# Optimization experiments

Measured on AMD Instinct MI355X. Metric: run time of the kernel, lower is better.

Reference implementation:

```python
import jax, jax.numpy as jnp
import numpy as np

FOCAL = 1015.0
IMG = 256


def setup_inputs() -> dict:
    key = jax.random.key(0)
    ks = jax.random.split(key, 9)
    B, NV, NF = 128, 35709, 70789
    coeff = jax.random.normal(ks[0], (B, 257), jnp.float32) * 0.1
    meanshape = jax.random.normal(ks[1], (NV * 3,), jnp.float32)
    idBase = jax.random.normal(ks[2], (NV * 3, 80), jnp.float32) * 0.01
    exBase = jax.random.normal(ks[3], (NV * 3, 64), jnp.float32) * 0.01
    meantex = jax.random.uniform(ks[4], (NV * 3,), jnp.float32) * 255.0
    texBase = jax.random.normal(ks[5], (NV * 3, 80), jnp.float32)
    # 1-based indices, matching the facemodel convention (code subtracts 1)
    tri = jax.random.randint(ks[6], (NF, 3), 1, NV + 1, jnp.int32)
    # point_buf may reference the appended zero face (index NF+1, 1-based)
    point_buf = jax.random.randint(ks[7], (NV, 8), 1, NF + 2, jnp.int32)
    kp_inds = jax.random.randint(ks[8], (68,), 0, NV, jnp.int32)
    return dict(coeff=coeff, meanshape=meanshape, idBase=idBase, exBase=exBase,
                meantex=meantex, texBase=texBase, tri=tri, point_buf=point_buf,
                kp_inds=kp_inds)


def _rotation(angles):
    # rotation = (Rz @ Ry @ Rx)^T, per Compute_rotation_matrix
    sx, sy, sz = jnp.sin(angles[:, 0]), jnp.sin(angles[:, 1]), jnp.sin(angles[:, 2])
    cx, cy, cz = jnp.cos(angles[:, 0]), jnp.cos(angles[:, 1]), jnp.cos(angles[:, 2])
    o, l = jnp.zeros_like(sx), jnp.ones_like(sx)
    Rx = jnp.stack([l, o, o, o, cx, -sx, o, sx, cx], -1).reshape(-1, 3, 3)
    Ry = jnp.stack([cy, o, sy, o, l, o, -sy, o, cy], -1).reshape(-1, 3, 3)
    Rz = jnp.stack([cz, -sz, o, sz, cz, o, o, o, l], -1).reshape(-1, 3, 3)
    return jnp.einsum('bij,bjk,bkl->bli', Rz, Ry, Rx)


def _compute_norm(shape, tri, point_buf):
    fid = tri - 1  # [F,3] 0-based vertex ids
    v1 = shape[:, fid[:, 0]]  # [B,F,3]
    v2 = shape[:, fid[:, 1]]
    v3 = shape[:, fid[:, 2]]
    fn = jnp.cross(v1 - v2, v2 - v3)  # per-face normals [B,F,3]
    fn = jnp.concatenate([fn, jnp.zeros_like(fn[:, :1])], axis=1)  # pad zero face
    vn = fn[:, point_buf - 1].sum(axis=2)  # [B,NV,8,3] -> [B,NV,3]
    return vn / jnp.linalg.norm(vn, axis=2, keepdims=True)


def _illumination(tex, norm, gamma):
    B, N, _ = tex.shape
    gamma = gamma.reshape(B, 3, 9).at[:, :, 0].add(0.8).transpose(0, 2, 1)  # [B,9,3]
    a0 = np.pi
    a1 = 2.0 * np.pi / np.sqrt(3.0)
    a2 = 2.0 * np.pi / np.sqrt(8.0)
    c0 = 1.0 / np.sqrt(4.0 * np.pi)
    c1 = np.sqrt(3.0) / np.sqrt(4.0 * np.pi)
    c2 = 3.0 * np.sqrt(5.0) / np.sqrt(12.0 * np.pi)
    d0 = 0.5 / np.sqrt(3.0)
    nx, ny, nz = norm[..., 0], norm[..., 1], norm[..., 2]
    Y = jnp.stack([
        jnp.full_like(nx, np.float32(a0 * c0)),
        -a1 * c1 * ny,
        a1 * c1 * nz,
        -a1 * c1 * nx,
        a2 * c2 * nx * ny,
        -a2 * c2 * ny * nz,
        a2 * c2 * d0 * (3.0 * nz ** 2 - 1.0),
        -a2 * c2 * nx * nz,
        a2 * c2 * 0.5 * (nx ** 2 - ny ** 2),
    ], axis=-1)  # [B,N,9]
    lighting = jnp.einsum('bnc,bcd->bnd', Y, gamma)  # [B,N,3]
    return tex * lighting


def _project(pts):
    half = IMG // 2
    pts = pts * jnp.array([1.0, 1.0, -1.0], jnp.float32) + jnp.array([0.0, 0.0, 10.0], jnp.float32)
    P = jnp.array([[FOCAL, 0.0, half], [0.0, FOCAL, half], [0.0, 0.0, 1.0]], jnp.float32)
    aug = pts @ P.T
    return aug[..., :2] / aug[..., 2:3]


def reference(coeff, meanshape, idBase, exBase, meantex, texBase, tri, point_buf, kp_inds):
    B = coeff.shape[0]
    idc, exc, texc = coeff[:, :80], coeff[:, 80:144], coeff[:, 144:224]
    angles, gamma, trans = coeff[:, 224:227], coeff[:, 227:254], coeff[:, 254:257]
    # Shape_formation
    shape = (idc @ idBase.T + exc @ exBase.T + meanshape).reshape(B, -1, 3)
    shape = shape - meanshape.reshape(1, -1, 3).mean(axis=1, keepdims=True)
    # Texture_formation
    tex = (texc @ texBase.T + meantex).reshape(B, -1, 3)
    # Normals, rotation, rigid transform
    vnorm = _compute_norm(shape, tri, point_buf)
    rot = _rotation(angles)  # [B,3,3]
    vnorm_r = jnp.einsum('bnc,bcd->bnd', vnorm, rot)
    shape_t = jnp.einsum('bnc,bcd->bnd', shape, rot) + trans[:, None, :]
    # Illumination (vertex colors) and landmark projection
    face_color = _illumination(tex, vnorm_r, gamma)
    lms = _project(shape_t[:, kp_inds])
    lms = jnp.stack([lms[..., 0], IMG - lms[..., 1]], axis=-1)
    return face_color, lms, shape_t
```

## Files before the change

kernel.cpp:

```cpp
#include <hip/hip_runtime.h>

typedef unsigned short u16;
typedef unsigned int u32;
typedef __attribute__((ext_vector_type(8))) short bfrag;
typedef __attribute__((ext_vector_type(4))) float ffrag;
typedef __attribute__((ext_vector_type(4))) float f4;
typedef __attribute__((ext_vector_type(2))) float f2;
typedef __attribute__((ext_vector_type(2))) u32 u32x2;
typedef __attribute__((ext_vector_type(4))) int i4;

#define NVERT 35709
#define NFACE 70789
#define NV3   107127
#define NB    128

#define SHAPE_OFF 0ull
#define TEX4_OFF  54849024ull
#define FXY_OFF   91415040ull
#define FZ_OFF    127659008ull
#define CPACK_OFF 145780992ull
#define MPAD_OFF  145846528ull
#define GG_OFF    145852672ull
#define MEAN_OFF  145866496ull
#define PART_OFF  145866512ull

#define LMS_BASE  13712256ull
#define ST_BASE   13729664ull

__device__ __forceinline__ float b2f(u16 s) {
  union { unsigned u; float f; } v; v.u = ((unsigned)s) << 16; return v.f;
}
__device__ __forceinline__ u16 f2b(float x) {
  union { float f; unsigned u; } v; v.f = x;
  unsigned r = v.u + 0x7FFFu + ((v.u >> 16) & 1u);
  return (u16)(r >> 16);
}
__device__ __forceinline__ u16 h2b(float x) {
  union { _Float16 h; u16 u; } v; v.h = (_Float16)x; return v.u;
}
__device__ __forceinline__ float hb2f(u16 u) {
  union { _Float16 h; u16 u2; } v; v.u2 = u; return (float)v.h;
}
__device__ __forceinline__ f4 ld4u(const float* p) {
  f4 r; __builtin_memcpy(&r, p, 16); return r;
}
__device__ __forceinline__ bfrag cvt8nt(const float* p) {
  f4 a = __builtin_nontemporal_load((const f4*)p);
  f4 b = __builtin_nontemporal_load((const f4*)(p + 4));
  bfrag r;
  r[0] = (short)f2b(a.x); r[1] = (short)f2b(a.y); r[2] = (short)f2b(a.z); r[3] = (short)f2b(a.w);
  r[4] = (short)f2b(b.x); r[5] = (short)f2b(b.y); r[6] = (short)f2b(b.z); r[7] = (short)f2b(b.w);
  return r;
}

__global__ __launch_bounds__(256) void k_mean(const float* __restrict__ ms, float* __restrict__ part) {
  __shared__ float s[3];
  if (threadIdx.x < 3) s[threadIdx.x] = 0.f;
  __syncthreads();
  float a0 = 0.f, a1 = 0.f, a2 = 0.f;
  for (int v = blockIdx.x * 256 + threadIdx.x; v < NVERT; v += 64 * 256) {
    a0 += ms[v * 3 + 0];
    a1 += ms[v * 3 + 1];
    a2 += ms[v * 3 + 2];
  }
  atomicAdd(&s[0], a0); atomicAdd(&s[1], a1); atomicAdd(&s[2], a2);
  __syncthreads();
  if (threadIdx.x < 3) part[blockIdx.x * 3 + threadIdx.x] = s[threadIdx.x];
}

__global__ __launch_bounds__(128) void k_params(const float* __restrict__ coeff, u16* __restrict__ cpack,
                                                float* __restrict__ mpad, float* __restrict__ G,
                                                const float* __restrict__ part, float* __restrict__ mean) {
  int b = threadIdx.x;
  if (b < 3) {
    float s = 0.f;
    for (int i = 0; i < 64; i++) s += part[i * 3 + b];
    mean[b] = s * (1.0f / (float)NVERT);
  }
  const float* c = coeff + b * 257;
  u16* cp = cpack + b * 256;
  for (int k = 0; k < 80; k++) cp[k] = f2b(c[k]);
  for (int k = 80; k < 96; k++) cp[k] = 0;
  for (int k = 0; k < 64; k++) cp[96 + k] = f2b(c[80 + k]);
  for (int k = 0; k < 80; k++) cp[160 + k] = f2b(c[144 + k]);
  for (int k = 240; k < 256; k++) cp[k] = 0;
  float ax = c[224], ay = c[225], az = c[226];
  float sx = sinf(ax), cx = cosf(ax);
  float sy = sinf(ay), cy = cosf(ay);
  float sz = sinf(az), cz = cosf(az);
  float* mp = mpad + b * 12;
  mp[0] = cz * cy;  mp[1] = cz * sy * sx - sz * cx;  mp[2] = sz * sx + cz * sy * cx;
  mp[3] = sz * cy;  mp[4] = cz * cx + sz * sy * sx;  mp[5] = sz * sy * cx - cz * sx;
  mp[6] = -sy;      mp[7] = cy * sx;                 mp[8] = cy * cx;
  mp[9] = c[254]; mp[10] = c[255]; mp[11] = c[256];
  float* g = G + b * 27;
  for (int cc = 0; cc < 9; cc++)
    for (int d = 0; d < 3; d++)
      g[cc * 3 + d] = c[227 + d * 9 + cc] + (cc == 0 ? 0.8f : 0.0f);
}

#define SBLK 558
__global__ __launch_bounds__(256) void k_gemmS(const float* __restrict__ idB, const float* __restrict__ exB,
                                               const float* __restrict__ ms, const u16* __restrict__ cpack,
                                               const float* __restrict__ meanc, const float* __restrict__ mpad,
                                               float* __restrict__ shp, float* __restrict__ out) {
  __shared__ float SW[4][2][384];
  int wave = threadIdx.x >> 6, lane = threadIdx.x & 63;
  int col = lane & 15, quad = lane >> 4;
  int jb = (blockIdx.x * 4 + wave) * 48;
  bfrag z8 = {0, 0, 0, 0, 0, 0, 0, 0};
  bfrag bid[3][3], bex[3][2];
  float msj[3], mcv[3];
#pragma unroll
  for (int T = 0; T < 3; T++) {
    int j = jb + T * 16 + col;
    int jc = j < NV3 ? j : NV3 - 1;
    const float* rowI = idB + (size_t)jc * 80;
    const float* rowE = exB + (size_t)jc * 64;
#pragma unroll
    for (int f = 0; f < 3; f++) {
      int k = f * 32 + quad * 8;
      bool ok = (k < 80);
      int ks = ok ? k : 0;
      bfrag vi = cvt8nt(rowI + ks);
      bid[T][f] = ok ? vi : z8;
    }
#pragma unroll
    for (int f = 0; f < 2; f++) bex[T][f] = cvt8nt(rowE + f * 32 + quad * 8);
    msj[T] = ms[jc];
    mcv[T] = meanc[jc % 3];
  }
  float (*SWl)[384] = SW[wave];
  int s0 = quad >> 1;
  int rb = (quad & 1) << 2;
  int vb = jb / 3;
  int ilim = NV3 - jb; ilim = (ilim > 48 ? 48 : ilim) * 8;
  int vlim = NVERT - vb; vlim = vlim > 16 ? 16 : vlim;

  for (int bt = 0; bt < 8; bt++) {
    const u16* cp = cpack + (size_t)(bt * 16 + col) * 256;
#pragma unroll
    for (int T = 0; T < 3; T++) {
      ffrag acc = {0.f, 0.f, 0.f, 0.f};
#pragma unroll
      for (int f = 0; f < 3; f++) {
        bfrag a = *(const bfrag*)(cp + f * 32 + quad * 8);
        acc = __builtin_amdgcn_mfma_f32_16x16x32_bf16(a, bid[T][f], acc, 0, 0, 0);
      }
#pragma unroll
      for (int f = 0; f < 2; f++) {
        bfrag a = *(const bfrag*)(cp + 96 + f * 32 + quad * 8);
        acc = __builtin_amdgcn_mfma_f32_16x16x32_bf16(a, bex[T][f], acc, 0, 0, 0);
      }
#pragma unroll
      for (int rr = 0; rr < 2; rr++) {
        f2 v2;
        v2.x = acc[2 * rr] + msj[T] - mcv[T];
        v2.y = acc[2 * rr + 1] + msj[T] - mcv[T];
        *(f2*)&SWl[s0][(T * 16 + col) * 8 + rb + 2 * rr] = v2;
      }
    }
#pragma unroll
    for (int s = 0; s < 2; s++) {
      size_t sb = (size_t)(bt * 2 + s) * (size_t)(NV3 * 8) + (size_t)jb * 8;
#pragma unroll
      for (int it = 0; it < 3; it++) {
        int i = it * 128 + lane * 2;
        if (i < ilim) {
          f2 vv = *(f2*)&SWl[s][i];
          __builtin_nontemporal_store(vv, (f2*)(shp + sb + i));
        }
      }
    }
#pragma unroll
    for (int s = 0; s < 2; s++) {
#pragma unroll
      for (int kk = 0; kk < 2; kk++) {
        int bi = (lane >> 4) + (kk << 2);
        int vloc = lane & 15;
        int b = bt * 16 + s * 8 + bi;
        float x = SWl[s][vloc * 24 + bi];
        float y = SWl[s][vloc * 24 + 8 + bi];
        float z = SWl[s][vloc * 24 + 16 + bi];
        const float* mp = mpad + b * 12;
        f4 m0 = *(const f4*)mp;
        f4 m1 = *(const f4*)(mp + 4);
        f4 m2 = *(const f4*)(mp + 8);
        if (vloc < vlim) {
          float ox = x * m0.x + y * m0.y + z * m0.z + m2.y;
          float oy = x * m0.w + y * m1.x + z * m1.y + m2.z;
          float oz = x * m1.z + y * m1.w + z * m2.x + m2.w;
          size_t o = ST_BASE + (size_t)b * NV3 + (size_t)(vb + vloc) * 3;
          __builtin_nontemporal_store(ox, out + o);
          __builtin_nontemporal_store(oy, out + o + 1);
          __builtin_nontemporal_store(oz, out + o + 2);
        }
      }
    }
  }
}

__global__ __launch_bounds__(256) void k_gemmT(const float* __restrict__ txB, const float* __restrict__ mt,
                                               const u16* __restrict__ cpack, u32* __restrict__ tex4) {
  __shared__ u16 TW[4][2][384];
  int wave = threadIdx.x >> 6, lane = threadIdx.x & 63;
  int col = lane & 15, quad = lane >> 4;
  int jb = (blockIdx.x * 4 + wave) * 48;
  bfrag z8 = {0, 0, 0, 0, 0, 0, 0, 0};
  bfrag btx[3][3];
  float mtj[3];
#pragma unroll
  for (int T = 0; T < 3; T++) {
    int j = jb + T * 16 + col;
    int jc = j < NV3 ? j : NV3 - 1;
    const float* rowT = txB + (size_t)jc * 80;
#pragma unroll
    for (int f = 0; f < 3; f++) {
      int k = f * 32 + quad * 8;
      bool ok = (k < 80);
      int ks = ok ? k : 0;
      bfrag vt = cvt8nt(rowT + ks);
      btx[T][f] = ok ? vt : z8;
    }
    mtj[T] = mt[jc];
  }
  u16 (*TWl)[384] = TW[wave];
  int s0 = quad >> 1;
  int rb = (quad & 1) << 2;
  int vb = jb / 3;
  int vlim = NVERT - vb; vlim = vlim > 16 ? 16 : vlim;

  for (int bt = 0; bt < 8; bt++) {
    const u16* cp = cpack + (size_t)(bt * 16 + col) * 256;
#pragma unroll
    for (int T = 0; T < 3; T++) {
      ffrag acc = {0.f, 0.f, 0.f, 0.f};
#pragma unroll
      for (int f = 0; f < 3; f++) {
        bfrag a = *(const bfrag*)(cp + 160 + f * 32 + quad * 8);
        acc = __builtin_amdgcn_mfma_f32_16x16x32_bf16(a, btx[T][f], acc, 0, 0, 0);
      }
#pragma unroll
      for (int rr = 0; rr < 2; rr++) {
        TWl[s0][(T * 16 + col) * 8 + rb + 2 * rr]     = f2b(acc[2 * rr] + mtj[T]);
        TWl[s0][(T * 16 + col) * 8 + rb + 2 * rr + 1] = f2b(acc[2 * rr + 1] + mtj[T]);
      }
    }
#pragma unroll
    for (int s = 0; s < 2; s++) {
#pragma unroll
      for (int kk = 0; kk < 2; kk++) {
        int bi = (lane >> 4) + (kk << 2);
        int vloc = lane & 15;
        if (vloc < vlim) {
          u16 x = TWl[s][(vloc * 3 + 0) * 8 + bi];
          u16 y = TWl[s][(vloc * 3 + 1) * 8 + bi];
          u16 z = TWl[s][(vloc * 3 + 2) * 8 + bi];
          u32x2 val;
          val.x = (u32)x | ((u32)y << 16);
          val.y = (u32)z;
          size_t idx = (((size_t)(bt * 2 + s) * NVERT + (vb + vloc)) * 8 + bi) * 2;
          __builtin_nontemporal_store(val, (u32x2*)(tex4 + idx));
        }
      }
    }
  }
}

#define FN_CH2 2213
__global__ __launch_bounds__(256) void k_fn(const float* __restrict__ shpT, const int* __restrict__ tri,
                                            u32* __restrict__ fxy, u16* __restrict__ fz, int lo) {
  int g = blockIdx.x;
  int xcd = g & 7, chunk = g >> 3;
  int bt8 = lo + xcd;
  int t = threadIdx.x;
  int bi = t & 7, foff = t >> 3;
  int f = chunk * 32 + foff;
  if (f >= NFACE) return;
  int i0 = tri[f * 3 + 0] - 1;
  int i1 = tri[f * 3 + 1] - 1;
  int i2 = tri[f * 3 + 2] - 1;
  const float* sl = shpT + (size_t)bt8 * (size_t)(NV3 * 8);
  int a0 = i0 * 24 + bi, a1 = i1 * 24 + bi, a2 = i2 * 24 + bi;
  float x1 = sl[a0], y1 = sl[a0 + 8], z1 = sl[a0 + 16];
  float x2 = sl[a1], y2 = sl[a1 + 8], z2 = sl[a1 + 16];
  float x3 = sl[a2], y3 = sl[a2 + 8], z3 = sl[a2 + 16];
  float e1x = x1 - x2, e1y = y1 - y2, e1z = z1 - z2;
  float e2x = x2 - x3, e2y = y2 - y3, e2z = z2 - z3;
  u16 hx = h2b(e1y * e2z - e1z * e2y);
  u16 hy = h2b(e1z * e2x - e1x * e2z);
  u16 hz = h2b(e1x * e2y - e1y * e2x);
  size_t o = (size_t)bt8 * (size_t)(NFACE * 8) + (size_t)f * 8 + bi;
  fxy[o] = (u32)hx | ((u32)hy << 16);
  fz[o] = hz;
}

#define FI_CH2 1116
__global__ __launch_bounds__(256) void k_final(const u32* __restrict__ tex4, const u32* __restrict__ fxy,
                                               const u16* __restrict__ fz, const int* __restrict__ pbuf,
                                               const float* __restrict__ mpad, const float* __restrict__ G,
                                               float* __restrict__ out, int lo) {
  __shared__ float scol[8][100];
  int g = blockIdx.x;
  int xcd = g & 7, chunk = g >> 3;
  int bt8 = lo + xcd;
  int t = threadIdx.x;
  int bi = t & 7, voff = t >> 3;
  int v0 = chunk * 32;
  int v = v0 + voff;
  int vc = v < NVERT ? v : NVERT - 1;
  bool valid = v < NVERT;
  int b = bt8 * 8 + bi;
  i4 p0 = *(const i4*)(pbuf + (size_t)vc * 8);
  i4 p1 = *(const i4*)(pbuf + (size_t)vc * 8 + 4);
  int idx[8] = {p0.x, p0.y, p0.z, p0.w, p1.x, p1.y, p1.z, p1.w};
  const u32* fx = fxy + (size_t)bt8 * (size_t)(NFACE * 8);
  const u16* fzb = fz + (size_t)bt8 * (size_t)(NFACE * 8);
  float vx = 0.f, vy = 0.f, vz = 0.f;
#pragma unroll
  for (int i = 0; i < 8; i++) {
    int id = idx[i] - 1;
    if (id < NFACE) {
      u32 q = fx[(size_t)id * 8 + bi];
      u16 qz = fzb[(size_t)id * 8 + bi];
      vx += hb2f((u16)q); vy += hb2f((u16)(q >> 16)); vz += hb2f(qz);
    }
  }
  float n2 = vx * vx + vy * vy + vz * vz;
  float inv = rsqrtf(fmaxf(n2, 1e-30f));
  vx *= inv; vy *= inv; vz *= inv;
  const float* mp = mpad + b * 12;
  f4 m0 = *(const f4*)mp;
  f4 m1 = *(const f4*)(mp + 4);
  float m8 = mp[8];
  float nx = vx * m0.x + vy * m0.y + vz * m0.z;
  float ny = vx * m0.w + vy * m1.x + vz * m1.y;
  float nz = vx * m1.z + vy * m1.w + vz * m8;
  const float kc1 = 1.7724539f;
  const float kc2 = 2.4270324f;
  const float kd0 = 0.28867513f;
  float Y[9];
  Y[0] = 0.8862269f;
  Y[1] = -kc1 * ny;
  Y[2] = kc1 * nz;
  Y[3] = -kc1 * nx;
  Y[4] = kc2 * nx * ny;
  Y[5] = -kc2 * ny * nz;
  Y[6] = kc2 * kd0 * (3.f * nz * nz - 1.f);
  Y[7] = -kc2 * nx * nz;
  Y[8] = kc2 * 0.5f * (nx * nx - ny * ny);
  const float* gg = G + b * 27;
  float gv[28];
#pragma unroll
  for (int q = 0; q < 7; q++) {
    f4 g4 = ld4u(gg + q * 4);
    gv[q * 4] = g4.x; gv[q * 4 + 1] = g4.y; gv[q * 4 + 2] = g4.z; gv[q * 4 + 3] = g4.w;
  }
  if (valid) {
    u32x2 tv = __builtin_nontemporal_load(
        (const u32x2*)(tex4 + ((size_t)bt8 * NVERT + vc) * 16 + bi * 2));
    float tc[3] = { b2f((u16)tv.x), b2f((u16)(tv.x >> 16)), b2f((u16)tv.y) };
#pragma unroll
    for (int d = 0; d < 3; d++) {
      float L = 0.f;
#pragma unroll
      for (int cc = 0; cc < 9; cc++) L += Y[cc] * gv[cc * 3 + d];
      scol[bi][voff * 3 + d] = tc[d] * L;
    }
  }
  __syncthreads();
  int nvv = NVERT - v0;
  int lim = (nvv < 32 ? nvv : 32) * 3;
  size_t base = (size_t)(bt8 * 8) * NV3 + (size_t)v0 * 3;
#pragma unroll
  for (int it = 0; it < 3; it++) {
    int l = it * 256 + t;
    int b2 = l / 96, e = l - b2 * 96;
    if (e < lim) {
      size_t o = base + (size_t)b2 * NV3 + e;
      __builtin_nontemporal_store(scol[b2][e], out + o);
    }
  }
}

__global__ __launch_bounds__(128) void k_lms(const float* __restrict__ shpT, const int* __restrict__ kp,
                                             const float* __restrict__ mpad, float* __restrict__ out) {
  int t = threadIdx.x;
  int b = blockIdx.x;
  if (t >= 68) return;
  int v = kp[t];
  const float* sl = shpT + (size_t)(b >> 3) * (size_t)(NV3 * 8) + (size_t)v * 24 + (b & 7);
  float sx = sl[0], sy = sl[8], sz = sl[16];
  const float* mp = mpad + b * 12;
  f4 m0 = *(const f4*)mp;
  f4 m1 = *(const f4*)(mp + 4);
  f4 m2 = *(const f4*)(mp + 8);
  float ox = sx * m0.x + sy * m0.y + sz * m0.z + m2.y;
  float oy = sx * m0.w + sy * m1.x + sz * m1.y + m2.z;
  float oz = sx * m1.z + sy * m1.w + sz * m2.x + m2.w;
  float w = 10.f - oz;
  float invw = 1.0f / w;
  float lx = 1015.f * ox * invw + 128.f;
  float ly = 1015.f * oy * invw + 128.f;
  size_t o = LMS_BASE + ((size_t)b * 68 + t) * 2;
  out[o + 0] = lx;
  out[o + 1] = 256.f - ly;
}

extern "C" void kernel_launch(void* const* d_in, const int* in_sizes, int n_in,
                              void* d_out, int out_size, void* d_ws, size_t ws_size,
                              hipStream_t stream) {
  const float* coeff     = (const float*)d_in[0];
  const float* meanshape = (const float*)d_in[1];
  const float* idB       = (const float*)d_in[2];
  const float* exB       = (const float*)d_in[3];
  const float* meantex   = (const float*)d_in[4];
  const float* txB       = (const float*)d_in[5];
  const int* tri         = (const int*)d_in[6];
  const int* pbuf        = (const int*)d_in[7];
  const int* kp          = (const int*)d_in[8];
  float* out = (float*)d_out;
  char* ws = (char*)d_ws;
  float* shpT = (float*)(ws + SHAPE_OFF);
  u32* tex4   = (u32*)(ws + TEX4_OFF);
  u32* fxy    = (u32*)(ws + FXY_OFF);
  u16* fzp    = (u16*)(ws + FZ_OFF);
  u16* cpack  = (u16*)(ws + CPACK_OFF);
  float* mpad = (float*)(ws + MPAD_OFF);
  float* G    = (float*)(ws + GG_OFF);
  float* mean = (float*)(ws + MEAN_OFF);
  float* part = (float*)(ws + PART_OFF);

  k_mean<<<64, 256, 0, stream>>>(meanshape, part);
  k_params<<<1, 128, 0, stream>>>(coeff, cpack, mpad, G, part, mean);
  k_gemmS<<<SBLK, 256, 0, stream>>>(idB, exB, meanshape, cpack, mean, mpad, shpT, out);
  k_gemmT<<<SBLK, 256, 0, stream>>>(txB, meantex, cpack, tex4);
  for (int lo = 0; lo < 16; lo += 8) {
    k_fn<<<8 * FN_CH2, 256, 0, stream>>>(shpT, tri, fxy, fzp, lo);
    k_final<<<8 * FI_CH2, 256, 0, stream>>>(tex4, fxy, fzp, pbuf, mpad, G, out, lo);
  }
  k_lms<<<128, 128, 0, stream>>>(shpT, kp, mpad, out);
}
```

Baseline: 434.4 us.

## Split GEMM batch loop across two block sets and pad LDS staging stride

The shape and texture GEMM kernels now launch twice as many blocks, and each block handles half of the batch tiles. This raises parallelism beyond 558 blocks on a large CU count, but each basis tile is now loaded and converted twice. The LDS staging rows are padded from 8 to 10 elements to reduce bank conflicts on the transposed reads. The basis loads switch from nontemporal to normal cached loads so the second split can hit in cache.

```diff
diff --git a/kernel.cpp b/kernel.cpp
--- a/kernel.cpp
+++ b/kernel.cpp
@@ -44,9 +44,9 @@
 __device__ __forceinline__ f4 ld4u(const float* p) {
   f4 r; __builtin_memcpy(&r, p, 16); return r;
 }
-__device__ __forceinline__ bfrag cvt8nt(const float* p) {
-  f4 a = __builtin_nontemporal_load((const f4*)p);
-  f4 b = __builtin_nontemporal_load((const f4*)(p + 4));
+__device__ __forceinline__ bfrag cvt8c(const float* p) {
+  f4 a = *(const f4*)p;
+  f4 b = *(const f4*)(p + 4);
   bfrag r;
   r[0] = (short)f2b(a.x); r[1] = (short)f2b(a.y); r[2] = (short)f2b(a.z); r[3] = (short)f2b(a.w);
   r[4] = (short)f2b(b.x); r[5] = (short)f2b(b.y); r[6] = (short)f2b(b.z); r[7] = (short)f2b(b.w);
@@ -104,10 +104,11 @@
                                                const float* __restrict__ ms, const u16* __restrict__ cpack,
                                                const float* __restrict__ meanc, const float* __restrict__ mpad,
                                                float* __restrict__ shp, float* __restrict__ out) {
-  __shared__ float SW[4][2][384];
+  __shared__ float SW[4][2][480];
+  int jblk = blockIdx.x % SBLK, split = blockIdx.x / SBLK;
   int wave = threadIdx.x >> 6, lane = threadIdx.x & 63;
   int col = lane & 15, quad = lane >> 4;
-  int jb = (blockIdx.x * 4 + wave) * 48;
+  int jb = (jblk * 4 + wave) * 48;
   bfrag z8 = {0, 0, 0, 0, 0, 0, 0, 0};
   bfrag bid[3][3], bex[3][2];
   float msj[3], mcv[3];
@@ -122,22 +123,22 @@
       int k = f * 32 + quad * 8;
       bool ok = (k < 80);
       int ks = ok ? k : 0;
-      bfrag vi = cvt8nt(rowI + ks);
+      bfrag vi = cvt8c(rowI + ks);
       bid[T][f] = ok ? vi : z8;
     }
 #pragma unroll
-    for (int f = 0; f < 2; f++) bex[T][f] = cvt8nt(rowE + f * 32 + quad * 8);
+    for (int f = 0; f < 2; f++) bex[T][f] = cvt8c(rowE + f * 32 + quad * 8);
     msj[T] = ms[jc];
     mcv[T] = meanc[jc % 3];
   }
-  float (*SWl)[384] = SW[wave];
+  float (*SWl)[480] = SW[wave];
   int s0 = quad >> 1;
   int rb = (quad & 1) << 2;
   int vb = jb / 3;
   int ilim = NV3 - jb; ilim = (ilim > 48 ? 48 : ilim) * 8;
   int vlim = NVERT - vb; vlim = vlim > 16 ? 16 : vlim;
 
-  for (int bt = 0; bt < 8; bt++) {
+  for (int bt = split * 4; bt < split * 4 + 4; bt++) {
     const u16* cp = cpack + (size_t)(bt * 16 + col) * 256;
 #pragma unroll
     for (int T = 0; T < 3; T++) {
@@ -157,7 +158,7 @@
         f2 v2;
         v2.x = acc[2 * rr] + msj[T] - mcv[T];
         v2.y = acc[2 * rr + 1] + msj[T] - mcv[T];
-        *(f2*)&SWl[s0][(T * 16 + col) * 8 + rb + 2 * rr] = v2;
+        *(f2*)&SWl[s0][(T * 16 + col) * 10 + rb + 2 * rr] = v2;
       }
     }
 #pragma unroll
@@ -167,7 +168,7 @@
       for (int it = 0; it < 3; it++) {
         int i = it * 128 + lane * 2;
         if (i < ilim) {
-          f2 vv = *(f2*)&SWl[s][i];
+          f2 vv = *(f2*)&SWl[s][(i >> 3) * 10 + (i & 7)];
           __builtin_nontemporal_store(vv, (f2*)(shp + sb + i));
         }
       }
@@ -179,9 +180,9 @@
         int bi = (lane >> 4) + (kk << 2);
         int vloc = lane & 15;
         int b = bt * 16 + s * 8 + bi;
-        float x = SWl[s][vloc * 24 + bi];
-        float y = SWl[s][vloc * 24 + 8 + bi];
-        float z = SWl[s][vloc * 24 + 16 + bi];
+        float x = SWl[s][vloc * 30 + bi];
+        float y = SWl[s][vloc * 30 + 10 + bi];
+        float z = SWl[s][vloc * 30 + 20 + bi];
         const float* mp = mpad + b * 12;
         f4 m0 = *(const f4*)mp;
         f4 m1 = *(const f4*)(mp + 4);
@@ -202,10 +203,11 @@
 
 __global__ __launch_bounds__(256) void k_gemmT(const float* __restrict__ txB, const float* __restrict__ mt,
                                                const u16* __restrict__ cpack, u32* __restrict__ tex4) {
-  __shared__ u16 TW[4][2][384];
+  __shared__ u16 TW[4][2][480];
+  int jblk = blockIdx.x % SBLK, split = blockIdx.x / SBLK;
   int wave = threadIdx.x >> 6, lane = threadIdx.x & 63;
   int col = lane & 15, quad = lane >> 4;
-  int jb = (blockIdx.x * 4 + wave) * 48;
+  int jb = (jblk * 4 + wave) * 48;
   bfrag z8 = {0, 0, 0, 0, 0, 0, 0, 0};
   bfrag btx[3][3];
   float mtj[3];
@@ -219,18 +221,18 @@
       int k = f * 32 + quad * 8;
       bool ok = (k < 80);
       int ks = ok ? k : 0;
-      bfrag vt = cvt8nt(rowT + ks);
+      bfrag vt = cvt8c(rowT + ks);
       btx[T][f] = ok ? vt : z8;
     }
     mtj[T] = mt[jc];
   }
-  u16 (*TWl)[384] = TW[wave];
+  u16 (*TWl)[480] = TW[wave];
   int s0 = quad >> 1;
   int rb = (quad & 1) << 2;
   int vb = jb / 3;
   int vlim = NVERT - vb; vlim = vlim > 16 ? 16 : vlim;
 
-  for (int bt = 0; bt < 8; bt++) {
+  for (int bt = split * 4; bt < split * 4 + 4; bt++) {
     const u16* cp = cpack + (size_t)(bt * 16 + col) * 256;
 #pragma unroll
     for (int T = 0; T < 3; T++) {
@@ -242,8 +244,8 @@
       }
 #pragma unroll
       for (int rr = 0; rr < 2; rr++) {
-        TWl[s0][(T * 16 + col) * 8 + rb + 2 * rr]     = f2b(acc[2 * rr] + mtj[T]);
-        TWl[s0][(T * 16 + col) * 8 + rb + 2 * rr + 1] = f2b(acc[2 * rr + 1] + mtj[T]);
+        TWl[s0][(T * 16 + col) * 10 + rb + 2 * rr]     = f2b(acc[2 * rr] + mtj[T]);
+        TWl[s0][(T * 16 + col) * 10 + rb + 2 * rr + 1] = f2b(acc[2 * rr + 1] + mtj[T]);
       }
     }
 #pragma unroll
@@ -253,9 +255,9 @@
         int bi = (lane >> 4) + (kk << 2);
         int vloc = lane & 15;
         if (vloc < vlim) {
-          u16 x = TWl[s][(vloc * 3 + 0) * 8 + bi];
-          u16 y = TWl[s][(vloc * 3 + 1) * 8 + bi];
-          u16 z = TWl[s][(vloc * 3 + 2) * 8 + bi];
+          u16 x = TWl[s][vloc * 30 + bi];
+          u16 y = TWl[s][vloc * 30 + 10 + bi];
+          u16 z = TWl[s][vloc * 30 + 20 + bi];
           u32x2 val;
           val.x = (u32)x | ((u32)y << 16);
           val.y = (u32)z;
@@ -433,8 +435,8 @@
 
   k_mean<<<64, 256, 0, stream>>>(meanshape, part);
   k_params<<<1, 128, 0, stream>>>(coeff, cpack, mpad, G, part, mean);
-  k_gemmS<<<SBLK, 256, 0, stream>>>(idB, exB, meanshape, cpack, mean, mpad, shpT, out);
-  k_gemmT<<<SBLK, 256, 0, stream>>>(txB, meantex, cpack, tex4);
+  k_gemmS<<<2 * SBLK, 256, 0, stream>>>(idB, exB, meanshape, cpack, mean, mpad, shpT, out);
+  k_gemmT<<<2 * SBLK, 256, 0, stream>>>(txB, meantex, cpack, tex4);
   for (int lo = 0; lo < 16; lo += 8) {
     k_fn<<<8 * FN_CH2, 256, 0, stream>>>(shpT, tri, fxy, fzp, lo);
     k_final<<<8 * FI_CH2, 256, 0, stream>>>(tex4, fxy, fzp, pbuf, mpad, G, out, lo);
```

Result: faster. 423.4 us (-2.5%).
